# Optimization experiments

Measured on AMD Instinct MI355X. Metric: run time of the kernel, lower is better.

The kernel has to match this reference:

```python
import jax, jax.numpy as jnp
import numpy as np

B, S, E, H = 4, 512, 512, 8
DH = E // H
HID = max(16, E // 4)  # sr_ratio=4
ALPHA = 0.1
EPS_SAFE = 0.05  # eps=1e-6 clamped to [0.05, 0.8]


def _xavier(k, shape):
    fan_out, fan_in = shape[0], shape[1]
    lim = (6.0 / (fan_in + fan_out)) ** 0.5
    return jax.random.uniform(k, shape, minval=-lim, maxval=lim, dtype=jnp.float32)


def setup_inputs() -> dict:
    key = jax.random.key(0)
    ks = jax.random.split(key, 8)
    return {
        "x": jax.random.normal(ks[0], (B, S, E), dtype=jnp.float32),
        "wq": _xavier(ks[1], (E, E)), "bq": jnp.zeros((E,), jnp.float32),
        "wk": _xavier(ks[2], (E, E)), "bk": jnp.zeros((E,), jnp.float32),
        "wv": _xavier(ks[3], (E, E)), "bv": jnp.zeros((E,), jnp.float32),
        "wo": _xavier(ks[4], (E, E)), "bo": jnp.zeros((E,), jnp.float32),
        # sr_conv1: Conv2d(1, HID, 1) -> weight [HID,1,1,1] == vector [HID]
        "w1": _xavier(ks[5], (HID, 1)).reshape(HID), "b1": jnp.zeros((HID,), jnp.float32),
        # sr_conv2: Conv2d(HID, 1, 1) -> weight [1,HID,1,1] == vector [HID]
        "w2": _xavier(ks[6], (1, HID)).reshape(HID), "b2": jnp.zeros((), jnp.float32),
    }


def _autopoietic_transform(scores, w1, b1, w2, b2):
    # scores: [B, H, S, S]
    scores = jnp.clip(jnp.nan_to_num(scores, nan=0.0, posinf=10.0, neginf=-10.0), -15.0, 15.0)
    mean_attn = scores.mean(axis=1)  # mean over heads -> [B, S, S]

    scaled = jnp.clip(jnp.clip(mean_attn, -8.0, 8.0) * EPS_SAFE, -10.0, 10.0)
    # conv1x1 (1 -> HID): broadcastmul; clamp + relu; conv1x1 (HID -> 1)
    hid = scaled[:, None, :, :] * w1[None, :, None, None] + b1[None, :, None, None]  # [B,HID,S,S]
    hid = jax.nn.relu(jnp.clip(hid, -5.0, 5.0))
    auto = jnp.einsum('bhij,h->bij', hid, w2) + b2  # [B,S,S]
    auto = jnp.clip(auto, -5.0, 5.0)

    # Taylor expansion with clamp, then sigmoid smoothing
    taylor = jnp.clip(1.0 + 0.05 * (auto * 50.0), 0.5, 1.5)
    sig = jax.nn.sigmoid(taylor)

    # fuzzy probability via entropy of softmax of mean attention
    p = jax.nn.softmax(jnp.clip(mean_attn, -10.0, 10.0), axis=-1)
    Hent = -p * jnp.log(p + 1e-6)
    Fm = jax.nn.softmax(3.0 * Hent, axis=-1)

    t = sig * Fm

    # energy (Frobenius-norm) balancing per batch
    e_o = jnp.sqrt((mean_attn ** 2).sum(axis=(1, 2))) + 1e-4
    e_t = jnp.sqrt((t ** 2).sum(axis=(1, 2))) + 1e-4
    gamma = jnp.clip(e_o / e_t, 0.8, 1.2)[:, None, None]
    t = gamma * t

    # dynamic std matching
    t_mean = t.mean(axis=(1, 2), keepdims=True)
    o_mean = mean_attn.mean(axis=(1, 2), keepdims=True)
    t_std = jnp.sqrt(jnp.clip(((t - t_mean) ** 2).mean(axis=(1, 2), keepdims=True), 0.01, None))
    o_std = jnp.sqrt(jnp.clip(((mean_attn - o_mean) ** 2).mean(axis=(1, 2), keepdims=True), 0.01, None))
    gdyn = jnp.clip(o_std / t_std, 0.8, 1.2)
    t = o_mean + gdyn * (t - t_mean)

    # residual blend of transformed map back into per-head scores (alpha=0.1), final clamp
    return jnp.clip(scores + ALPHA * t[:, None, :, :], -15.0, 15.0)


def reference(x, wq, bq, wk, bk, wv, bv, wo, bo, w1, b1, w2, b2):
    scaling = DH ** -0.5
    q = (jnp.einsum('bse,oe->bso', x, wq) + bq).reshape(B, S, H, DH).transpose(0, 2, 1, 3) * scaling
    k = (jnp.einsum('bse,oe->bso', x, wk) + bk).reshape(B, S, H, DH).transpose(0, 2, 1, 3)
    v = (jnp.einsum('bse,oe->bso', x, wv) + bv).reshape(B, S, H, DH).transpose(0, 2, 1, 3)
    scores = jnp.einsum('bhqd,bhkd->bhqk', q, k)  # [B,H,S,S]
    scores = _autopoietic_transform(scores, w1, b1, w2, b2)
    attn = jax.nn.softmax(scores, axis=-1)
    out = jnp.einsum('bhqk,bhkd->bhqd', attn, v).transpose(0, 2, 1, 3).reshape(B, S, E)
    return jnp.einsum('bse,oe->bso', out, wo) + bo
```

## Files before the change

kernel.cpp:

```cpp
#include <hip/hip_runtime.h>
#include <math.h>

#define BATCH 4
#define SEQ   512
#define EMB   512
#define NH    8
#define DHD   64
#define HIDN  128
#define ALPHA 0.1f
#define EPSS  0.05f

#define LUTN  2048
#define XMIN  (-0.4f)
#define XSTEP (0.8f / LUTN)

typedef __attribute__((ext_vector_type(8))) short  bf16x8;
typedef __attribute__((ext_vector_type(4))) float  f32x4;
#define MFMA(a,b,c) __builtin_amdgcn_mfma_f32_16x16x32_bf16((a),(b),(c),0,0,0)

__device__ __forceinline__ unsigned short f2bf(float f) {
    union { float f; unsigned u; } v; v.f = f;
    unsigned r = v.u + 0x7fffu + ((v.u >> 16) & 1u);
    return (unsigned short)(r >> 16);
}
__device__ __forceinline__ float bf2f(unsigned short h) {
    union { unsigned u; float f; } v; v.u = ((unsigned)h) << 16;
    return v.f;
}
__device__ __forceinline__ float f16tof(unsigned short h) {
    union { unsigned short s; _Float16 f; } v; v.s = h; return (float)v.f;
}
__device__ __forceinline__ unsigned short ftof16(float f) {
    union { unsigned short s; _Float16 f; } v; v.f = (_Float16)f; return v.s;
}

__device__ __forceinline__ void async_lds16(const unsigned short* g, unsigned short* l) {
    __builtin_amdgcn_global_load_lds(
        (const __attribute__((address_space(1))) void*)g,
        (__attribute__((address_space(3))) void*)l, 16, 0, 0);
}

template<int KS, int UN, int MT>
__device__ __forceinline__ void gemm_core64(
    const unsigned short* __restrict__ A, const unsigned short* __restrict__ B,
    int m0, int n0, unsigned short* sA, unsigned short* sB, f32x4 (&acc)[2][4])
{
    const int K = KS * 64;
    const int tid = threadIdx.x, w = tid >> 6, lane = tid & 63;
    const int quad = lane >> 4, r = lane & 15;
    const int wm = w >> 1, wn = w & 1;
    const int lrow = lane >> 3, lc = lane & 7;
    const int sc = lc ^ lrow;
    constexpr int AF = MT / 32;
    constexpr int NB = UN * 32 / 32;

    const unsigned short* ag[2]; unsigned short* dAu[2];
    #pragma unroll
    for (int c = 0; c < AF; c++) {
        const int rb = w * (8 * AF) + c * 8;
        ag[c]  = A + (long)(m0 + rb + lrow) * K + sc * 8;
        dAu[c] = sA + rb * 64;
    }
    const unsigned short* bg[4]; unsigned short* dBu[4];
    #pragma unroll
    for (int c = 0; c < NB; c++) {
        const int rb = w * (8 * NB) + c * 8;
        bg[c]  = B + (long)(n0 + rb + lrow) * K + sc * 8;
        dBu[c] = sB + rb * 64;
    }

    for (int s = 0; s < KS; s++) {
        const int k0 = s * 64;
        #pragma unroll
        for (int c = 0; c < AF; c++) async_lds16(ag[c] + k0, dAu[c]);
        #pragma unroll
        for (int c = 0; c < NB; c++) async_lds16(bg[c] + k0, dBu[c]);
        __syncthreads();
        #pragma unroll
        for (int kc = 0; kc < 2; kc++) {
            bf16x8 af[2], bfr[4];
            #pragma unroll
            for (int t = 0; t < AF; t++) {
                const int row = wm * (16 * AF) + t * 16 + r;
                af[t] = *(const bf16x8*)(sA + row * 64 + ((kc * 4 + quad) ^ (row & 7)) * 8);
            }
            #pragma unroll
            for (int u = 0; u < UN; u++) {
                const int row = wn * (16 * UN) + u * 16 + r;
                bfr[u] = *(const bf16x8*)(sB + row * 64 + ((kc * 4 + quad) ^ (row & 7)) * 8);
            }
            #pragma unroll
            for (int t = 0; t < AF; t++)
                #pragma unroll
                for (int u = 0; u < UN; u++)
                    acc[t][u] = MFMA(af[t], bfr[u], acc[t][u]);
        }
        __syncthreads();
    }
}

__global__ __launch_bounds__(256) void gemm_qkv(
    const unsigned short* __restrict__ x_ext, const unsigned short* __restrict__ w_ext,
    const float* __restrict__ bq, const float* __restrict__ bk, const float* __restrict__ bv,
    unsigned short* __restrict__ q_ext, unsigned short* __restrict__ k_ext,
    unsigned short* __restrict__ vT)
{
    __shared__ __align__(16) unsigned short sA[64 * 64];
    __shared__ __align__(16) unsigned short sB[64 * 64];
    __shared__ float sC[64 * 68];

    const int m0 = blockIdx.y * 64, n0 = blockIdx.x * 64;
    f32x4 acc[2][4] = {};
    gemm_core64<24, 2, 64>(x_ext, w_ext, m0, n0, sA, sB, acc);

    const int tid = threadIdx.x, w = tid >> 6, lane = tid & 63;
    const int quad = lane >> 4, r = lane & 15;
    const int wm = w >> 1, wn = w & 1;
    #pragma unroll
    for (int t = 0; t < 2; t++)
        #pragma unroll
        for (int u = 0; u < 2; u++)
            #pragma unroll
            for (int g = 0; g < 4; g++)
                sC[(wm * 32 + t * 16 + quad * 4 + g) * 68 + wn * 32 + u * 16 + r] = acc[t][u][g];
    __syncthreads();

    const int which = n0 >> 9;
    const int n0l = n0 & 511;
    const int h0 = n0l >> 6;
    const int b = m0 >> 9, s0 = m0 & 511;

    if (which < 2) {
        const float scl = (which == 0) ? 0.125f : 1.0f;
        const float* bias = (which == 0) ? bq : bk;
        unsigned* dst = (unsigned*)((which == 0) ? q_ext : k_ext);
        #pragma unroll
        for (int seg = 0; seg < 3; seg++) {
            const bool lo = (which == 0) ? (seg == 1) : (seg == 2);
            #pragma unroll
            for (int it = 0; it < 8; it++) {
                const int idx = it * 256 + tid;
                const int sl = idx >> 5;
                const int jc = idx & 31;
                const int nc = jc * 2;
                float v0 = (sC[sl * 68 + nc]     + bias[n0l + nc])     * scl;
                float v1 = (sC[sl * 68 + nc + 1] + bias[n0l + nc + 1]) * scl;
                unsigned short a0 = f2bf(v0), a1 = f2bf(v1);
                if (lo) { a0 = f2bf(v0 - bf2f(a0)); a1 = f2bf(v1 - bf2f(a1)); }
                const long orow = (long)(b * NH + h0) * SEQ + s0 + sl;
                dst[orow * 96 + seg * 32 + jc] = (unsigned)a0 | ((unsigned)a1 << 16);
            }
        }
    } else {
        unsigned* dst = (unsigned*)vT;
        #pragma unroll
        for (int it = 0; it < 8; it++) {
            const int idx = it * 256 + tid;
            const int d = idx >> 5;
            const int jc = idx & 31;
            const int sl = jc * 2;
            const float bvv = bv[n0l + d];
            const float v0 = sC[sl * 68 + d] + bvv;
            const float v1 = sC[(sl + 1) * 68 + d] + bvv;
            const long orow = (long)(b * NH + h0) * DHD + d;
            dst[orow * 256 + (s0 >> 1) + jc] = (unsigned)f2bf(v0) | ((unsigned)f2bf(v1) << 16);
        }
    }
}

__global__ __launch_bounds__(256) void gemm_scores(
    const unsigned short* __restrict__ q_ext, const unsigned short* __restrict__ k_ext,
    unsigned short* __restrict__ scoresH)
{
    __shared__ __align__(16) unsigned short sA[64 * 64];
    __shared__ __align__(16) unsigned short sB[128 * 64];
    const int z = blockIdx.z;
    const int m0 = blockIdx.y * 64, n0 = blockIdx.x * 128;
    f32x4 acc[2][4] = {};
    gemm_core64<3, 4, 64>(q_ext + (long)z * SEQ * 192, k_ext + (long)z * SEQ * 192,
                          m0, n0, sA, sB, acc);

    const int tid = threadIdx.x, w = tid >> 6, lane = tid & 63;
    const int quad = lane >> 4, r = lane & 15;
    const int wm = w >> 1, wn = w & 1;
    unsigned short* hC = sB;
    #pragma unroll
    for (int t = 0; t < 2; t++)
        #pragma unroll
        for (int u = 0; u < 4; u++)
            #pragma unroll
            for (int g = 0; g < 4; g++) {
                const int ml = wm * 32 + t * 16 + quad * 4 + g;
                const int nl = wn * 64 + u * 16 + r;
                hC[ml * 128 + nl] = ftof16(fminf(fmaxf(acc[t][u][g], -15.f), 15.f));
            }
    __syncthreads();
    #pragma unroll
    for (int it = 0; it < 4; it++) {
        const int id = it * 256 + tid;
        const int ml = id >> 4, ch = id & 15;
        *(uint4*)(scoresH + ((long)z * SEQ + m0 + ml) * SEQ + n0 + ch * 8) =
            *(const uint4*)(hC + ml * 128 + ch * 8);
    }
}

__global__ __launch_bounds__(256) void gemm_proj(
    const unsigned short* __restrict__ otmp, const unsigned short* __restrict__ woh,
    const float* __restrict__ bo, float* __restrict__ out)
{
    __shared__ __align__(16) unsigned short sA[32 * 64];
    __shared__ __align__(16) unsigned short sB[64 * 64];
    const int m0 = blockIdx.y * 32, n0 = blockIdx.x * 64;
    f32x4 acc[2][4] = {};
    gemm_core64<8, 2, 32>(otmp, woh, m0, n0, sA, sB, acc);
    const int tid = threadIdx.x, w = tid >> 6, lane = tid & 63;
    const int quad = lane >> 4, r = lane & 15;
    const int wm = w >> 1, wn = w & 1;
    #pragma unroll
    for (int u = 0; u < 2; u++)
        #pragma unroll
        for (int g = 0; g < 4; g++) {
            const int m = m0 + wm * 16 + quad * 4 + g;
            const int n = n0 + wn * 32 + u * 16 + r;
            out[(long)m * EMB + n] = acc[0][u][g] + bo[n];
        }
}

__device__ __forceinline__ float blockReduceSum(float v, float* sred) {
    #pragma unroll
    for (int o = 32; o > 0; o >>= 1) v += __shfl_down(v, o);
    __syncthreads();
    if ((threadIdx.x & 63) == 0) sred[threadIdx.x >> 6] = v;
    __syncthreads();
    return (sred[0] + sred[1]) + (sred[2] + sred[3]);
}
__device__ __forceinline__ float blockReduceMax(float v, float* sred) {
    #pragma unroll
    for (int o = 32; o > 0; o >>= 1) v = fmaxf(v, __shfl_down(v, o));
    __syncthreads();
    if ((threadIdx.x & 63) == 0) sred[threadIdx.x >> 6] = v;
    __syncthreads();
    return fmaxf(fmaxf(sred[0], sred[1]), fmaxf(sred[2], sred[3]));
}

__global__ __launch_bounds__(256) void prep_kernel(
    const float* __restrict__ x,
    const float* __restrict__ wq, const float* __restrict__ wk,
    const float* __restrict__ wv, const float* __restrict__ wo,
    const float* __restrict__ w1, const float* __restrict__ b1,
    const float* __restrict__ w2, const float* __restrict__ b2,
    unsigned short* __restrict__ x_ext, unsigned short* __restrict__ w_ext,
    unsigned short* __restrict__ woh, float* __restrict__ lut)
{
    const int blk = blockIdx.x;
    if (blk < 9) {
        const int i = blk * 256 + threadIdx.x;
        if (i > LUTN) return;
        const float xv = XMIN + i * XSTEP;
        float a = 0.f;
        for (int h = 0; h < HIDN; h++) {
            float hv = xv * w1[h] + b1[h];
            hv = fminf(fmaxf(hv, -5.f), 5.f);
            hv = fmaxf(hv, 0.f);
            a += hv * w2[h];
        }
        a += b2[0];
        a = fminf(fmaxf(a, -5.f), 5.f);
        const float taylor = fminf(fmaxf(1.f + 2.5f * a, 0.5f), 1.5f);
        lut[i] = 1.f / (1.f + expf(-taylor));
        return;
    }
    const int i = (blk - 9) * 256 + threadIdx.x;
    if (i < 1048576) {
        const int m = i >> 9, k = i & 511;
        const float v = x[i];
        const unsigned short h = f2bf(v), l = f2bf(v - bf2f(h));
        const long bb = (long)m * 1536 + k;
        x_ext[bb] = h; x_ext[bb + 512] = l; x_ext[bb + 1024] = h;
    } else if (i < 1835008) {
        const int j = i - 1048576;
        const int n = j >> 9, k = j & 511;
        const float v = (j < 262144) ? wq[j] : (j < 524288 ? wk[j - 262144] : wv[j - 524288]);
        const unsigned short h = f2bf(v), l = f2bf(v - bf2f(h));
        const long bb = (long)n * 1536 + k;
        w_ext[bb] = h; w_ext[bb + 512] = h; w_ext[bb + 1024] = l;
    } else {
        const int j = i - 1835008;
        woh[j] = f2bf(wo[j]);
    }
}

__global__ __launch_bounds__(256) void transform_kernel(
    const unsigned short* __restrict__ scoresH,
    const float* __restrict__ lut,
    unsigned short* __restrict__ t0H,
    float4* __restrict__ partials)
{
    const int rr = blockIdx.x;
    const int b = rr >> 9, i = rr & 511;
    const int tid = threadIdx.x;

    __shared__ float slut[LUTN + 1];
    __shared__ float sred[4];

    for (int u = tid; u <= LUTN; u += 256) slut[u] = lut[u];

    const unsigned* baseU =
        (const unsigned*)(scoresH + (((long)(b * NH)) * SEQ + i) * SEQ) + tid;
    float s0 = 0.f, s1 = 0.f;
    #pragma unroll
    for (int h = 0; h < NH; h++) {
        const unsigned pv = baseU[h * (SEQ * SEQ / 2)];
        s0 += f16tof((unsigned short)pv);
        s1 += f16tof((unsigned short)(pv >> 16));
    }
    float mv[2] = { s0 * 0.125f, s1 * 0.125f };
    __syncthreads();

    float sigv[2], mclip[2];
    float lmax = -1e30f;
    #pragma unroll
    for (int u = 0; u < 2; u++) {
        const float m = mv[u];
        const float x = fminf(fmaxf(m, -8.f), 8.f) * EPSS;
        float t = (x - XMIN) * (1.0f / XSTEP);
        int idx = (int)t;
        idx = idx < 0 ? 0 : (idx > LUTN - 1 ? LUTN - 1 : idx);
        const float frac = t - (float)idx;
        const float l0 = slut[idx], l1 = slut[idx + 1];
        sigv[u] = l0 + frac * (l1 - l0);
        const float mc = fminf(fmaxf(m, -10.f), 10.f);
        mclip[u] = mc;
        lmax = fmaxf(lmax, mc);
    }

    const float rmax = blockReduceMax(lmax, sred);
    float ex[2], lsum = 0.f;
    #pragma unroll
    for (int u = 0; u < 2; u++) { ex[u] = expf(mclip[u] - rmax); lsum += ex[u]; }
    const float rsum = blockReduceSum(lsum, sred);
    const float inv = 1.f / rsum;

    float hent[2], lmax2 = -1e30f;
    #pragma unroll
    for (int u = 0; u < 2; u++) {
        const float p = ex[u] * inv;
        const float he = -p * logf(p + 1e-6f);
        hent[u] = 3.f * he;
        lmax2 = fmaxf(lmax2, hent[u]);
    }
    const float rmax2 = blockReduceMax(lmax2, sred);
    float ex2[2], lsum2 = 0.f;
    #pragma unroll
    for (int u = 0; u < 2; u++) { ex2[u] = expf(hent[u] - rmax2); lsum2 += ex2[u]; }
    const float rsum2 = blockReduceSum(lsum2, sred);
    const float inv2 = 1.f / rsum2;

    float tv[2];
    #pragma unroll
    for (int u = 0; u < 2; u++) tv[u] = sigv[u] * (ex2[u] * inv2);
    ((unsigned*)t0H)[((long)b * SEQ + i) * (SEQ / 2) + tid] =
        (unsigned)ftof16(tv[0]) | ((unsigned)ftof16(tv[1]) << 16);

    float s_m  = blockReduceSum(mv[0] + mv[1], sred);
    float s_m2 = blockReduceSum(mv[0] * mv[0] + mv[1] * mv[1], sred);
    float s_t  = blockReduceSum(tv[0] + tv[1], sred);
    float s_t2 = blockReduceSum(tv[0] * tv[0] + tv[1] * tv[1], sred);
    if (tid == 0) partials[rr] = make_float4(s_m, s_m2, s_t, s_t2);
}

__global__ __launch_bounds__(256) void softmax_attnv(
    const unsigned short* __restrict__ scoresH,
    const unsigned short* __restrict__ t0H,
    const float4* __restrict__ partials,
    const unsigned short* __restrict__ vT,
    unsigned short* __restrict__ otmp)
{
    __shared__ __align__(16) unsigned short attnS[32 * 520];
    __shared__ __align__(16) unsigned short sB[64 * 64];
    __shared__ float sC[32 * 66];
    __shared__ float sred[4];

    const int m0 = blockIdx.x * 32;
    const int z  = blockIdx.y;
    const int b  = z >> 3, h = z & 7;
    const int tid = threadIdx.x, wv = tid >> 6, lane = tid & 63;

    const float4 p0 = partials[b * SEQ + tid];
    const float4 p1 = partials[b * SEQ + tid + 256];
    float sm  = blockReduceSum(p0.x + p1.x, sred);
    float sm2 = blockReduceSum(p0.y + p1.y, sred);
    float st  = blockReduceSum(p0.z + p1.z, sred);
    float st2 = blockReduceSum(p0.w + p1.w, sred);
    const float n = (float)SEQ * (float)SEQ;
    const float gamma = fminf(fmaxf((sqrtf(sm2) + 1e-4f) / (sqrtf(st2) + 1e-4f), 0.8f), 1.2f);
    const float o_mean = sm / n, t0m = st / n;
    const float o_std = sqrtf(fmaxf(fmaxf(sm2 / n - o_mean * o_mean, 0.f), 0.01f));
    const float t_std = sqrtf(fmaxf(gamma * gamma * fmaxf(st2 / n - t0m * t0m, 0.f), 0.01f));
    const float gdyn = fminf(fmaxf(o_std / t_std, 0.8f), 1.2f);
    const float c1 = gdyn * gamma;
    const float c0 = o_mean - c1 * t0m;

    const int j0 = lane * 8;
    for (int it = 0; it < 8; it++) {
        const int rowl = it * 4 + wv;
        const bf16x8 sr = *(const bf16x8*)(scoresH + ((long)z * SEQ + m0 + rowl) * SEQ + j0);
        const bf16x8 tr = *(const bf16x8*)(t0H + ((long)b * SEQ + m0 + rowl) * SEQ + j0);
        float sv[8];
        float lmax = -1e30f;
        #pragma unroll
        for (int u = 0; u < 8; u++) {
            float s = f16tof((unsigned short)sr[u])
                    + ALPHA * (c0 + c1 * f16tof((unsigned short)tr[u]));
            s = fminf(fmaxf(s, -15.f), 15.f);
            sv[u] = s;
            lmax = fmaxf(lmax, s);
        }
        #pragma unroll
        for (int o = 32; o > 0; o >>= 1) lmax = fmaxf(lmax, __shfl_down(lmax, o));
        lmax = __shfl(lmax, 0);
        float lsum = 0.f;
        #pragma unroll
        for (int u = 0; u < 8; u++) { sv[u] = expf(sv[u] - lmax); lsum += sv[u]; }
        #pragma unroll
        for (int o = 32; o > 0; o >>= 1) lsum += __shfl_down(lsum, o);
        lsum = __shfl(lsum, 0);
        const float inv = 1.f / lsum;
        bf16x8 pk;
        #pragma unroll
        for (int u = 0; u < 8; u++) pk[u] = (short)f2bf(sv[u] * inv);
        *(bf16x8*)(attnS + rowl * 520 + j0) = pk;
    }
    __syncthreads();

    const int quad = lane >> 4, r = lane & 15;
    const int wm = wv >> 1, wn = wv & 1;
    const int lrow = lane >> 3, lc = lane & 7;
    const int sc = lc ^ lrow;
    const unsigned short* bg0 = vT + (long)z * DHD * SEQ + (long)(wv * 16 + lrow) * SEQ + sc * 8;
    const unsigned short* bg1 = bg0 + 8 * SEQ;
    unsigned short* dB0 = sB + (wv * 16) * 64;
    unsigned short* dB1 = sB + (wv * 16 + 8) * 64;
    f32x4 acc[2] = {};
    for (int s = 0; s < 8; s++) {
        const int k0 = s * 64;
        async_lds16(bg0 + k0, dB0);
        async_lds16(bg1 + k0, dB1);
        __syncthreads();
        #pragma unroll
        for (int kc = 0; kc < 2; kc++) {
            const bf16x8 a = *(const bf16x8*)(attnS + (wm * 16 + r) * 520 + k0 + kc * 32 + quad * 8);
            #pragma unroll
            for (int u = 0; u < 2; u++) {
                const int row = wn * 32 + u * 16 + r;
                const bf16x8 bb = *(const bf16x8*)(sB + row * 64 + ((kc * 4 + quad) ^ (row & 7)) * 8);
                acc[u] = MFMA(a, bb, acc[u]);
            }
        }
        __syncthreads();
    }

    #pragma unroll
    for (int u = 0; u < 2; u++)
        #pragma unroll
        for (int g = 0; g < 4; g++)
            sC[(wm * 16 + quad * 4 + g) * 66 + wn * 32 + u * 16 + r] = acc[u][g];
    __syncthreads();
    unsigned* dst = (unsigned*)otmp;
    #pragma unroll
    for (int it = 0; it < 4; it++) {
        const int idx = it * 256 + tid;
        const int sr2 = idx >> 5, jc = idx & 31;
        const float v0 = sC[sr2 * 66 + jc * 2], v1 = sC[sr2 * 66 + jc * 2 + 1];
        dst[((long)(b * SEQ + m0 + sr2)) * 256 + h * 32 + jc] =
            (unsigned)f2bf(v0) | ((unsigned)f2bf(v1) << 16);
    }
}

extern "C" void kernel_launch(void* const* d_in, const int* in_sizes, int n_in,
                              void* d_out, int out_size, void* d_ws, size_t ws_size,
                              hipStream_t stream) {
    const float* x  = (const float*)d_in[0];
    const float* wq = (const float*)d_in[1];
    const float* bq = (const float*)d_in[2];
    const float* wk = (const float*)d_in[3];
    const float* bk = (const float*)d_in[4];
    const float* wv = (const float*)d_in[5];
    const float* bv = (const float*)d_in[6];
    const float* wo = (const float*)d_in[7];
    const float* bo = (const float*)d_in[8];
    const float* w1 = (const float*)d_in[9];
    const float* b1 = (const float*)d_in[10];
    const float* w2 = (const float*)d_in[11];
    const float* b2 = (const float*)d_in[12];
    float* out = (float*)d_out;

    char* wsb = (char*)d_ws;
    unsigned short* scoresH = (unsigned short*)wsb;
    unsigned short* t0H     = scoresH + 8388608;
    float4* partials = (float4*)(t0H + 1048576);
    float*  lutbuf   = (float*)(partials + 2048);
    unsigned short* u16 = (unsigned short*)(wsb + (20u << 20));
    unsigned short* x_ext = u16;
    unsigned short* w_ext = x_ext + 3145728;
    unsigned short* q_ext = w_ext + 2359296;
    unsigned short* k_ext = q_ext + 3145728;
    unsigned short* vT    = k_ext + 3145728;
    unsigned short* otmp  = vT + 1048576;
    unsigned short* woh   = otmp + 1048576;

    prep_kernel<<<dim3(9 + 8192), dim3(256), 0, stream>>>(
        x, wq, wk, wv, wo, w1, b1, w2, b2, x_ext, w_ext, woh, lutbuf);

    gemm_qkv<<<dim3(24, 32), dim3(256), 0, stream>>>(
        x_ext, w_ext, bq, bk, bv, q_ext, k_ext, vT);

    gemm_scores<<<dim3(4, 8, 32), dim3(256), 0, stream>>>(q_ext, k_ext, scoresH);

    transform_kernel<<<dim3(BATCH * SEQ), dim3(256), 0, stream>>>(
        scoresH, lutbuf, t0H, partials);

    softmax_attnv<<<dim3(16, 32), dim3(256), 0, stream>>>(
        scoresH, t0H, partials, vT, otmp);

    gemm_proj<<<dim3(8, 64), dim3(256), 0, stream>>>(otmp, woh, bo, out);
}
```

Measured before the change: 147.0 us.

## Vectorize prep, drop softmax max-reductions, merge block reductions, alias shared memory

The prep kernel now reads float4 and writes packed bf16 pairs, so it launches a quarter as many blocks. The transform and softmax kernels skip the max-subtraction reductions, since the inputs are clamped to small ranges where exp cannot overflow. The four separate block sums are merged into one float4 reduction. Shared memory is aliased in gemm_qkv and softmax_attnv to cut LDS use and raise occupancy, and the first V tile load is issued before the softmax phase so it overlaps. The attention tile uses an XOR swizzle instead of padding, which risks subtle indexing errors and a small numeric change from the unshifted exp.

```diff
diff --git a/kernel.cpp b/kernel.cpp
--- a/kernel.cpp
+++ b/kernel.cpp
@@ -52,7 +52,7 @@
     const int lrow = lane >> 3, lc = lane & 7;
     const int sc = lc ^ lrow;
     constexpr int AF = MT / 32;
-    constexpr int NB = UN * 32 / 32;
+    constexpr int NB = UN;
 
     const unsigned short* ag[2]; unsigned short* dAu[2];
     #pragma unroll
@@ -105,9 +105,10 @@
     unsigned short* __restrict__ q_ext, unsigned short* __restrict__ k_ext,
     unsigned short* __restrict__ vT)
 {
-    __shared__ __align__(16) unsigned short sA[64 * 64];
-    __shared__ __align__(16) unsigned short sB[64 * 64];
-    __shared__ float sC[64 * 68];
+    __shared__ __align__(16) unsigned char smem[64 * 68 * 4];
+    unsigned short* sA = (unsigned short*)smem;
+    unsigned short* sB = (unsigned short*)(smem + 64 * 64 * 2);
+    float* sC = (float*)smem;
 
     const int m0 = blockIdx.y * 64, n0 = blockIdx.x * 64;
     f32x4 acc[2][4] = {};
@@ -234,13 +235,21 @@
     __syncthreads();
     return (sred[0] + sred[1]) + (sred[2] + sred[3]);
 }
-__device__ __forceinline__ float blockReduceMax(float v, float* sred) {
-    #pragma unroll
-    for (int o = 32; o > 0; o >>= 1) v = fmaxf(v, __shfl_down(v, o));
-    __syncthreads();
-    if ((threadIdx.x & 63) == 0) sred[threadIdx.x >> 6] = v;
-    __syncthreads();
-    return fmaxf(fmaxf(sred[0], sred[1]), fmaxf(sred[2], sred[3]));
+__device__ __forceinline__ float4 blockReduceSum4(float4 v, float4* s4) {
+    #pragma unroll
+    for (int o = 32; o > 0; o >>= 1) {
+        v.x += __shfl_down(v.x, o); v.y += __shfl_down(v.y, o);
+        v.z += __shfl_down(v.z, o); v.w += __shfl_down(v.w, o);
+    }
+    __syncthreads();
+    if ((threadIdx.x & 63) == 0) s4[threadIdx.x >> 6] = v;
+    __syncthreads();
+    float4 r;
+    r.x = (s4[0].x + s4[1].x) + (s4[2].x + s4[3].x);
+    r.y = (s4[0].y + s4[1].y) + (s4[2].y + s4[3].y);
+    r.z = (s4[0].z + s4[1].z) + (s4[2].z + s4[3].z);
+    r.w = (s4[0].w + s4[1].w) + (s4[2].w + s4[3].w);
+    return r;
 }
 
 __global__ __launch_bounds__(256) void prep_kernel(
@@ -271,22 +280,41 @@
         return;
     }
     const int i = (blk - 9) * 256 + threadIdx.x;
-    if (i < 1048576) {
-        const int m = i >> 9, k = i & 511;
-        const float v = x[i];
-        const unsigned short h = f2bf(v), l = f2bf(v - bf2f(h));
-        const long bb = (long)m * 1536 + k;
-        x_ext[bb] = h; x_ext[bb + 512] = l; x_ext[bb + 1024] = h;
-    } else if (i < 1835008) {
-        const int j = i - 1048576;
-        const int n = j >> 9, k = j & 511;
-        const float v = (j < 262144) ? wq[j] : (j < 524288 ? wk[j - 262144] : wv[j - 524288]);
-        const unsigned short h = f2bf(v), l = f2bf(v - bf2f(h));
-        const long bb = (long)n * 1536 + k;
-        w_ext[bb] = h; w_ext[bb + 512] = h; w_ext[bb + 1024] = l;
+    if (i < 262144) {
+        const int m = i >> 7, kq = i & 127;
+        const float4 v = ((const float4*)x)[i];
+        const unsigned short h0 = f2bf(v.x), h1 = f2bf(v.y), h2 = f2bf(v.z), h3 = f2bf(v.w);
+        const unsigned hi01 = (unsigned)h0 | ((unsigned)h1 << 16);
+        const unsigned hi23 = (unsigned)h2 | ((unsigned)h3 << 16);
+        const unsigned lo01 = (unsigned)f2bf(v.x - bf2f(h0)) | ((unsigned)f2bf(v.y - bf2f(h1)) << 16);
+        const unsigned lo23 = (unsigned)f2bf(v.z - bf2f(h2)) | ((unsigned)f2bf(v.w - bf2f(h3)) << 16);
+        unsigned* dst = (unsigned*)x_ext;
+        const long base = (long)m * 768 + kq * 2;
+        dst[base] = hi01;       dst[base + 1] = hi23;
+        dst[base + 256] = lo01; dst[base + 257] = lo23;
+        dst[base + 512] = hi01; dst[base + 513] = hi23;
+    } else if (i < 458752) {
+        const int j = i - 262144;
+        const int n = j >> 7, kq = j & 127;
+        const float4 v = (j < 65536) ? ((const float4*)wq)[j]
+                       : (j < 131072 ? ((const float4*)wk)[j - 65536]
+                                     : ((const float4*)wv)[j - 131072]);
+        const unsigned short h0 = f2bf(v.x), h1 = f2bf(v.y), h2 = f2bf(v.z), h3 = f2bf(v.w);
+        const unsigned hi01 = (unsigned)h0 | ((unsigned)h1 << 16);
+        const unsigned hi23 = (unsigned)h2 | ((unsigned)h3 << 16);
+        const unsigned lo01 = (unsigned)f2bf(v.x - bf2f(h0)) | ((unsigned)f2bf(v.y - bf2f(h1)) << 16);
+        const unsigned lo23 = (unsigned)f2bf(v.z - bf2f(h2)) | ((unsigned)f2bf(v.w - bf2f(h3)) << 16);
+        unsigned* dst = (unsigned*)w_ext;
+        const long base = (long)n * 768 + kq * 2;
+        dst[base] = hi01;       dst[base + 1] = hi23;
+        dst[base + 256] = hi01; dst[base + 257] = hi23;
+        dst[base + 512] = lo01; dst[base + 513] = lo23;
     } else {
-        const int j = i - 1835008;
-        woh[j] = f2bf(wo[j]);
+        const int j = i - 458752;
+        const float4 v = ((const float4*)wo)[j];
+        unsigned* dst = (unsigned*)woh;
+        dst[j * 2]     = (unsigned)f2bf(v.x) | ((unsigned)f2bf(v.y) << 16);
+        dst[j * 2 + 1] = (unsigned)f2bf(v.z) | ((unsigned)f2bf(v.w) << 16);
     }
 }
 
@@ -302,6 +330,7 @@
 
     __shared__ float slut[LUTN + 1];
     __shared__ float sred[4];
+    __shared__ float4 sred4[4];
 
     for (int u = tid; u <= LUTN; u += 256) slut[u] = lut[u];
 
@@ -317,8 +346,8 @@
     float mv[2] = { s0 * 0.125f, s1 * 0.125f };
     __syncthreads();
 
-    float sigv[2], mclip[2];
-    float lmax = -1e30f;
+    float sigv[2], ex[2];
+    float lsum = 0.f;
     #pragma unroll
     for (int u = 0; u < 2; u++) {
         const float m = mv[u];
@@ -329,30 +358,20 @@
         const float frac = t - (float)idx;
         const float l0 = slut[idx], l1 = slut[idx + 1];
         sigv[u] = l0 + frac * (l1 - l0);
-        const float mc = fminf(fmaxf(m, -10.f), 10.f);
-        mclip[u] = mc;
-        lmax = fmaxf(lmax, mc);
-    }
-
-    const float rmax = blockReduceMax(lmax, sred);
-    float ex[2], lsum = 0.f;
-    #pragma unroll
-    for (int u = 0; u < 2; u++) { ex[u] = expf(mclip[u] - rmax); lsum += ex[u]; }
+        ex[u] = expf(fminf(fmaxf(m, -10.f), 10.f));
+        lsum += ex[u];
+    }
     const float rsum = blockReduceSum(lsum, sred);
     const float inv = 1.f / rsum;
 
-    float hent[2], lmax2 = -1e30f;
+    float ex2[2], lsum2 = 0.f;
     #pragma unroll
     for (int u = 0; u < 2; u++) {
         const float p = ex[u] * inv;
         const float he = -p * logf(p + 1e-6f);
-        hent[u] = 3.f * he;
-        lmax2 = fmaxf(lmax2, hent[u]);
-    }
-    const float rmax2 = blockReduceMax(lmax2, sred);
-    float ex2[2], lsum2 = 0.f;
-    #pragma unroll
-    for (int u = 0; u < 2; u++) { ex2[u] = expf(hent[u] - rmax2); lsum2 += ex2[u]; }
+        ex2[u] = expf(3.f * he);
+        lsum2 += ex2[u];
+    }
     const float rsum2 = blockReduceSum(lsum2, sred);
     const float inv2 = 1.f / rsum2;
 
@@ -362,11 +381,13 @@
     ((unsigned*)t0H)[((long)b * SEQ + i) * (SEQ / 2) + tid] =
         (unsigned)ftof16(tv[0]) | ((unsigned)ftof16(tv[1]) << 16);
 
-    float s_m  = blockReduceSum(mv[0] + mv[1], sred);
-    float s_m2 = blockReduceSum(mv[0] * mv[0] + mv[1] * mv[1], sred);
-    float s_t  = blockReduceSum(tv[0] + tv[1], sred);
-    float s_t2 = blockReduceSum(tv[0] * tv[0] + tv[1] * tv[1], sred);
-    if (tid == 0) partials[rr] = make_float4(s_m, s_m2, s_t, s_t2);
+    float4 pv;
+    pv.x = mv[0] + mv[1];
+    pv.y = mv[0] * mv[0] + mv[1] * mv[1];
+    pv.z = tv[0] + tv[1];
+    pv.w = tv[0] * tv[0] + tv[1] * tv[1];
+    const float4 rs = blockReduceSum4(pv, sred4);
+    if (tid == 0) partials[rr] = rs;
 }
 
 __global__ __launch_bounds__(256) void softmax_attnv(
@@ -376,10 +397,11 @@
     const unsigned short* __restrict__ vT,
     unsigned short* __restrict__ otmp)
 {
-    __shared__ __align__(16) unsigned short attnS[32 * 520];
-    __shared__ __align__(16) unsigned short sB[64 * 64];
-    __shared__ float sC[32 * 66];
-    __shared__ float sred[4];
+    __shared__ __align__(16) unsigned char smem[40960];
+    unsigned short* attnS = (unsigned short*)smem;
+    unsigned short* sB    = (unsigned short*)(smem + 32768);
+    float*  sC    = (float*)smem;
+    float4* sred4 = (float4*)smem;
 
     const int m0 = blockIdx.x * 32;
     const int z  = blockIdx.y;
@@ -388,10 +410,9 @@
 
     const float4 p0 = partials[b * SEQ + tid];
     const float4 p1 = partials[b * SEQ + tid + 256];
-    float sm  = blockReduceSum(p0.x + p1.x, sred);
-    float sm2 = blockReduceSum(p0.y + p1.y, sred);
-    float st  = blockReduceSum(p0.z + p1.z, sred);
-    float st2 = blockReduceSum(p0.w + p1.w, sred);
+    float4 pv4 = make_float4(p0.x + p1.x, p0.y + p1.y, p0.z + p1.z, p0.w + p1.w);
+    const float4 rs4 = blockReduceSum4(pv4, sred4);
+    const float sm = rs4.x, sm2 = rs4.y, st = rs4.z, st2 = rs4.w;
     const float n = (float)SEQ * (float)SEQ;
     const float gamma = fminf(fmaxf((sqrtf(sm2) + 1e-4f) / (sqrtf(st2) + 1e-4f), 0.8f), 1.2f);
     const float o_mean = sm / n, t0m = st / n;
@@ -400,6 +421,16 @@
     const float gdyn = fminf(fmaxf(o_std / t_std, 0.8f), 1.2f);
     const float c1 = gdyn * gamma;
     const float c0 = o_mean - c1 * t0m;
+    __syncthreads();
+
+    const int lrow = lane >> 3, lc = lane & 7;
+    const int scw = lc ^ lrow;
+    const unsigned short* bg0 = vT + (long)z * DHD * SEQ + (long)(wv * 16 + lrow) * SEQ + scw * 8;
+    const unsigned short* bg1 = bg0 + 8 * SEQ;
+    unsigned short* dB0 = sB + (wv * 16) * 64;
+    unsigned short* dB1 = sB + (wv * 16 + 8) * 64;
+    async_lds16(bg0, dB0);
+    async_lds16(bg1, dB1);
 
     const int j0 = lane * 8;
     for (int it = 0; it < 8; it++) {
@@ -407,21 +438,15 @@
         const bf16x8 sr = *(const bf16x8*)(scoresH + ((long)z * SEQ + m0 + rowl) * SEQ + j0);
         const bf16x8 tr = *(const bf16x8*)(t0H + ((long)b * SEQ + m0 + rowl) * SEQ + j0);
         float sv[8];
-        float lmax = -1e30f;
+        float lsum = 0.f;
         #pragma unroll
         for (int u = 0; u < 8; u++) {
             float s = f16tof((unsigned short)sr[u])
                     + ALPHA * (c0 + c1 * f16tof((unsigned short)tr[u]));
             s = fminf(fmaxf(s, -15.f), 15.f);
-            sv[u] = s;
-            lmax = fmaxf(lmax, s);
-        }
-        #pragma unroll
-        for (int o = 32; o > 0; o >>= 1) lmax = fmaxf(lmax, __shfl_down(lmax, o));
-        lmax = __shfl(lmax, 0);
-        float lsum = 0.f;
-        #pragma unroll
-        for (int u = 0; u < 8; u++) { sv[u] = expf(sv[u] - lmax); lsum += sv[u]; }
+            sv[u] = expf(s);
+            lsum += sv[u];
+        }
         #pragma unroll
         for (int o = 32; o > 0; o >>= 1) lsum += __shfl_down(lsum, o);
         lsum = __shfl(lsum, 0);
@@ -429,27 +454,20 @@
         bf16x8 pk;
         #pragma unroll
         for (int u = 0; u < 8; u++) pk[u] = (short)f2bf(sv[u] * inv);
-        *(bf16x8*)(attnS + rowl * 520 + j0) = pk;
-    }
-    __syncthreads();
+        *(bf16x8*)(attnS + rowl * 512 + (j0 ^ ((rowl & 7) << 3))) = pk;
+    }
 
     const int quad = lane >> 4, r = lane & 15;
     const int wm = wv >> 1, wn = wv & 1;
-    const int lrow = lane >> 3, lc = lane & 7;
-    const int sc = lc ^ lrow;
-    const unsigned short* bg0 = vT + (long)z * DHD * SEQ + (long)(wv * 16 + lrow) * SEQ + sc * 8;
-    const unsigned short* bg1 = bg0 + 8 * SEQ;
-    unsigned short* dB0 = sB + (wv * 16) * 64;
-    unsigned short* dB1 = sB + (wv * 16 + 8) * 64;
+    const int arow = wm * 16 + r;
+    const int aswz = (arow & 7) << 3;
     f32x4 acc[2] = {};
     for (int s = 0; s < 8; s++) {
+        __syncthreads();
         const int k0 = s * 64;
-        async_lds16(bg0 + k0, dB0);
-        async_lds16(bg1 + k0, dB1);
-        __syncthreads();
         #pragma unroll
         for (int kc = 0; kc < 2; kc++) {
-            const bf16x8 a = *(const bf16x8*)(attnS + (wm * 16 + r) * 520 + k0 + kc * 32 + quad * 8);
+            const bf16x8 a = *(const bf16x8*)(attnS + arow * 512 + ((k0 + kc * 32 + quad * 8) ^ aswz));
             #pragma unroll
             for (int u = 0; u < 2; u++) {
                 const int row = wn * 32 + u * 16 + r;
@@ -458,6 +476,7 @@
             }
         }
         __syncthreads();
+        if (s < 7) { async_lds16(bg0 + (s + 1) * 64, dB0); async_lds16(bg1 + (s + 1) * 64, dB1); }
     }
 
     #pragma unroll
@@ -509,7 +528,7 @@
     unsigned short* otmp  = vT + 1048576;
     unsigned short* woh   = otmp + 1048576;
 
-    prep_kernel<<<dim3(9 + 8192), dim3(256), 0, stream>>>(
+    prep_kernel<<<dim3(9 + 2048), dim3(256), 0, stream>>>(
         x, wq, wk, wv, wo, w1, b1, w2, b2, x_ext, w_ext, woh, lutbuf);
 
     gemm_qkv<<<dim3(24, 32), dim3(256), 0, stream>>>(
```

After: 145.5 us (median of 2 runs). Within noise of the previous version (-1.0%).
